# Optimization experiments

Measured on AMD Instinct MI355X. Metric: run time of the kernel, lower is better.

Reference implementation:

```python
import jax, jax.numpy as jnp
import numpy as np

N_TIME = 512          # n_time_nodes
LATENT = 32           # latent_dim
HIDDEN = 64           # hidden_dim
N_MODES = 8           # r_fourier_modes
X_A0 = 0.3            # initial stoichiometry (anode)
CSANMAX = 28700.0     # max concentration scale
BASE_LOGIT = float(np.log(X_A0 / (1.0 - X_A0)))  # logit_from_fraction(x_a0)
FEAT_DIM = 1 + 2 * N_MODES   # [rho, cos(k*pi*rho), sin(k*pi*rho)]
IN_DIM = LATENT + FEAT_DIM
N_POINTS = 2_000_000


def setup_inputs() -> dict:
    key = jax.random.key(0)
    ks = jax.random.split(key, 8)
    time_idx = jax.random.randint(ks[0], (N_POINTS,), 0, N_TIME)
    rho = jax.random.uniform(ks[1], (N_POINTS,), dtype=jnp.float32)
    # trainable latent code per nonzero time node
    emb = jax.random.normal(ks[2], (N_TIME - 1, LATENT), dtype=jnp.float32) * 0.02
    # decoder_a: Linear(IN,HID)+SiLU, Linear(HID,HID)+SiLU, Linear(HID,1)
    W0 = jax.random.normal(ks[3], (IN_DIM, HIDDEN), dtype=jnp.float32) / np.sqrt(IN_DIM)
    b0 = jnp.zeros((HIDDEN,), jnp.float32)
    W1 = jax.random.normal(ks[4], (HIDDEN, HIDDEN), dtype=jnp.float32) / np.sqrt(HIDDEN)
    b1 = jnp.zeros((HIDDEN,), jnp.float32)
    Wout = jax.random.normal(ks[5], (HIDDEN, 1), dtype=jnp.float32) * 0.1
    bout = jnp.zeros((1,), jnp.float32)
    return {"time_idx": time_idx, "rho": rho, "emb": emb,
            "W0": W0, "b0": b0, "W1": W1, "b1": b1, "Wout": Wout, "bout": bout}


def _radius_features(rho):
    # [N] -> [N, 1 + 2*N_MODES]
    k = jnp.arange(1, N_MODES + 1, dtype=rho.dtype)
    ang = jnp.pi * rho[:, None] * k[None, :]
    return jnp.concatenate([rho[:, None], jnp.cos(ang), jnp.sin(ang)], axis=1)


def reference(time_idx, rho, emb, W0, b0, W1, b1, Wout, bout):
    # predicated version of the torch masked scatter: compute everywhere,
    # select initial-condition value where time_idx == 0
    idx = jnp.clip(time_idx - 1, 0, N_TIME - 2)       # safe gather index
    e = emb[idx]                                       # [N, LATENT]
    feat = _radius_features(rho)                       # [N, FEAT_DIM]
    h = jnp.concatenate([e, feat], axis=1)             # [N, IN_DIM]
    h = jax.nn.silu(h @ W0 + b0)
    h = jax.nn.silu(h @ W1 + b1)
    raw = (h @ Wout + bout)[:, 0]                      # [N]
    theta = jax.nn.sigmoid(raw + BASE_LOGIT)
    return jnp.where(time_idx == 0, X_A0 * CSANMAX, theta * CSANMAX)
```

## Files before the change

kernel.cpp:

```cpp
#include <hip/hip_runtime.h>
#include <stdint.h>


typedef _Float16 half8  __attribute__((ext_vector_type(8)));
typedef _Float16 half4v __attribute__((ext_vector_type(4)));
typedef _Float16 half2v __attribute__((ext_vector_type(2)));
typedef float f32x4 __attribute__((ext_vector_type(4)));

#define LOG2E 1.44269504088896340736f
#define NLN2  -0.6931471805599453f
#define CSCL  -1.44269504088896340736f
#define BASE_LOGIT -0.84729786038720367f
#define CSANMAX 28700.0f
#define IC_VAL 8610.0f

__device__ __forceinline__ float fast_exp2(float x) { return __builtin_amdgcn_exp2f(x); }
__device__ __forceinline__ float fast_rcp(float x)  { return __builtin_amdgcn_rcpf(x); }
__device__ __forceinline__ void usilu2(float u0, float u1, float& p0, float& p1) {
  const float d0 = 1.0f + fast_exp2(u0);
  const float d1 = 1.0f + fast_exp2(u1);
  const float r  = fast_rcp(d0 * d1);
  p0 = u0 * d1 * r;
  p1 = u1 * d0 * r;
}
__device__ __forceinline__ half2v pkh(float a, float b) {
  return __builtin_bit_cast(half2v, __builtin_amdgcn_cvt_pkrtz(a, b));
}

union H8 { half8 v8; half2v v2[4]; half4v v4[2]; };
union H4 { half4v v4; half2v v2[2]; };

__global__ __launch_bounds__(256, 3) void mlp_kernel(
    const int* __restrict__ tix, const float* __restrict__ rho,
    const float* __restrict__ emb, const float* __restrict__ W0,
    const float* __restrict__ b0, const float* __restrict__ W1,
    const float* __restrict__ b1, const float* __restrict__ Wout,
    const float* __restrict__ bout, float* __restrict__ out, int ntiles)
{
  __shared__ __align__(16) _Float16 stage[2][2][4][64][8];

  const int tid  = threadIdx.x;
  const int wid  = tid >> 6;
  const int lane = tid & 63;
  const int m    = lane & 15;
  const int q    = lane >> 4;

  if (wid == 0) {
#pragma unroll
    for (int t = 0; t < 4; ++t) {
#pragma unroll
      for (int s = 0; s < 2; ++s) {
        half8 f0, f1;
#pragma unroll
        for (int j = 0; j < 8; ++j) {
          const int k = s * 32 + q * 8 + j;
          const int n = t * 16 + m;
          float v0;
          if (k < 32) {
            v0 = W0[k * 64 + n];
          } else {
            const int kn = k - 32;
            v0 = (kn < 16) ? W0[(33 + kn) * 64 + n]
               : (kn == 16) ? W0[32 * 64 + n]
               : (kn == 17) ? b0[n] : 0.0f;
          }
          f0[j] = (_Float16)(CSCL * v0);
          const int hm = (s * 2 + (j >> 2)) * 16 + q * 4 + (j & 3);
          f1[j] = (_Float16)W1[hm * 64 + n];
        }
        *(half8*)&stage[0][s][t][lane][0] = f0;
        *(half8*)&stage[1][s][t][lane][0] = f1;
      }
    }
  }

  half2v biash[8];
  half2v wouth[8];
#pragma unroll
  for (int t = 0; t < 4; ++t) {
    const f32x4 bv = *(const f32x4*)(b1 + t * 16 + q * 4);
    const f32x4 wv = *(const f32x4*)(Wout + t * 16 + q * 4);
    biash[t * 2]     = pkh(CSCL * bv[0], CSCL * bv[1]);
    biash[t * 2 + 1] = pkh(CSCL * bv[2], CSCL * bv[3]);
    wouth[t * 2]     = pkh(NLN2 * wv[0], NLN2 * wv[1]);
    wouth[t * 2 + 1] = pkh(NLN2 * wv[2], NLN2 * wv[3]);
  }
  const float boutBL = bout[0] + BASE_LOGIT;

  __syncthreads();

  half8 w0A[4], w0B[4], w1A[4], w1B[4];
#pragma unroll
  for (int t = 0; t < 4; ++t) {
    w0A[t] = *(const half8*)&stage[0][0][t][lane][0];
    w0B[t] = *(const half8*)&stage[0][1][t][lane][0];
    w1A[t] = *(const half8*)&stage[1][0][t][lane][0];
    w1B[t] = *(const half8*)&stage[1][1][t][lane][0];
  }

  const f32x4 z = {0.0f, 0.0f, 0.0f, 0.0f};
  const int S = gridDim.x * 4;

  int tg = blockIdx.x * 4 + wid;
  if (tg >= ntiles) return;
  const int lim = ntiles - 1;

  auto phase1 = [&](float rhp, half8 X0v, H8& Y0o, H8& Y1o) {
    const float rev = 0.5f * rhp;
    const float c1  = __builtin_amdgcn_cosf(rev);
    const float s1f = __builtin_amdgcn_sinf(rev);
    const float tc  = 2.0f * c1;
    const float x1v = (q == 0) ? c1 : ((q == 1) ? s1f : 0.0f);
    const float x0v = (q == 0) ? 1.0f : 0.0f;
    const float x2v = tc * x1v - x0v;
    const float x3v = tc * x2v - x1v;
    const float x4v = tc * x3v - x2v;
    const float x5v = tc * x4v - x3v;
    const float x6v = tc * x5v - x4v;
    const float x7v = tc * x6v - x5v;
    const float x8v = tc * x7v - x6v;
    H8 X1;
    X1.v2[0] = (q == 2) ? pkh(rhp, 1.0f) : pkh(x1v, x2v);
    X1.v2[1] = pkh(x3v, x4v);
    X1.v2[2] = pkh(x5v, x6v);
    X1.v2[3] = pkh(x7v, x8v);

    f32x4 acc[4];
#pragma unroll
    for (int t = 0; t < 4; ++t) {
      f32x4 a = __builtin_amdgcn_mfma_f32_16x16x32_f16(w0A[t], X0v, z, 0, 0, 0);
      a = __builtin_amdgcn_mfma_f32_16x16x32_f16(w0B[t], X1.v8, a, 0, 0, 0);
      acc[t] = a;
    }
    H4 hh[4];
#pragma unroll
    for (int t = 0; t < 4; ++t) {
      float p0, p1, p2, p3;
      usilu2(acc[t][0], acc[t][1], p0, p1);
      usilu2(acc[t][2], acc[t][3], p2, p3);
      hh[t].v2[0] = pkh(p0, p1);
      hh[t].v2[1] = pkh(p2, p3);
    }
    Y0o.v4[0] = hh[0].v4; Y0o.v4[1] = hh[1].v4;
    Y1o.v4[0] = hh[2].v4; Y1o.v4[1] = hh[3].v4;
  };

  auto phase2 = [&](const H8& Y0p, const H8& Y1p, int icP, int tgP) {
    f32x4 acc[4];
#pragma unroll
    for (int t = 0; t < 4; ++t) {
      f32x4 a = __builtin_amdgcn_mfma_f32_16x16x32_f16(w1A[t], Y0p.v8, z, 0, 0, 0);
      a = __builtin_amdgcn_mfma_f32_16x16x32_f16(w1B[t], Y1p.v8, a, 0, 0, 0);
      acc[t] = a;
    }
    float dA = 0.0f, dB = 0.0f;
#pragma unroll
    for (int t = 0; t < 4; ++t) {
      float p0, p1, p2, p3;
      const float u0 = (float)biash[t * 2][0]     + acc[t][0];
      const float u1 = (float)biash[t * 2][1]     + acc[t][1];
      const float u2 = (float)biash[t * 2 + 1][0] + acc[t][2];
      const float u3 = (float)biash[t * 2 + 1][1] + acc[t][3];
      usilu2(u0, u1, p0, p1);
      usilu2(u2, u3, p2, p3);
      dA = fmaf(p0, (float)wouth[t * 2][0],     dA);
      dB = fmaf(p1, (float)wouth[t * 2][1],     dB);
      dA = fmaf(p2, (float)wouth[t * 2 + 1][0], dA);
      dB = fmaf(p3, (float)wouth[t * 2 + 1][1], dB);
    }
    float dot = dA + dB;
    dot += __shfl_xor(dot, 16, 64);
    dot += __shfl_xor(dot, 32, 64);
    const float theta = fast_rcp(1.0f + fast_exp2(-LOG2E * (dot + boutBL)));
    const float val = (icP == 0) ? IC_VAL : theta * CSANMAX;
    if (q == 0) out[tgP * 16 + m] = val;
  };

  int   tC = tix[tg * 16 + m];
  float rC = rho[tg * 16 + m];
  const int tg1 = min(tg + S, lim);
  int   tN = tix[tg1 * 16 + m];
  float rN = rho[tg1 * 16 + m];
  H8 X0C;
  {
    const int idx = min(max(tC - 1, 0), 510);
    const float* e = emb + (size_t)idx * 32 + q * 8;
    const f32x4 e0 = *(const f32x4*)e;
    const f32x4 e1 = *(const f32x4*)(e + 4);
    X0C.v2[0] = pkh(e0[0], e0[1]); X0C.v2[1] = pkh(e0[2], e0[3]);
    X0C.v2[2] = pkh(e1[0], e1[1]); X0C.v2[3] = pkh(e1[2], e1[3]);
  }
  H8 Y0p, Y1p;
  phase1(rC, X0C.v8, Y0p, Y1p);
  int icP = tC, tgP = tg;
  {
    const int idx = min(max(tN - 1, 0), 510);
    const float* e = emb + (size_t)idx * 32 + q * 8;
    const f32x4 e0 = *(const f32x4*)e;
    const f32x4 e1 = *(const f32x4*)(e + 4);
    X0C.v2[0] = pkh(e0[0], e0[1]); X0C.v2[1] = pkh(e0[2], e0[3]);
    X0C.v2[2] = pkh(e1[0], e1[1]); X0C.v2[3] = pkh(e1[2], e1[3]);
  }
  tC = tN; rC = rN;
  {
    const int tg2 = min(tg + 2 * S, lim);
    tN = tix[tg2 * 16 + m];
    rN = rho[tg2 * 16 + m];
  }
  tg += S;

  while (tg < ntiles) {
    const int tg2 = min(tg + 2 * S, lim);
    const int   tQ = tix[tg2 * 16 + m];
    const float rQ = rho[tg2 * 16 + m];
    const int idxN = min(max(tN - 1, 0), 510);
    const float* ern = emb + (size_t)idxN * 32 + q * 8;
    const f32x4 eN0 = *(const f32x4*)ern;
    const f32x4 eN1 = *(const f32x4*)(ern + 4);

    phase2(Y0p, Y1p, icP, tgP);
    phase1(rC, X0C.v8, Y0p, Y1p);

    icP = tC; tgP = tg;
    X0C.v2[0] = pkh(eN0[0], eN0[1]); X0C.v2[1] = pkh(eN0[2], eN0[3]);
    X0C.v2[2] = pkh(eN1[0], eN1[1]); X0C.v2[3] = pkh(eN1[2], eN1[3]);
    tC = tN; rC = rN;
    tN = tQ; rN = rQ;
    tg += S;
  }

  phase2(Y0p, Y1p, icP, tgP);
}

extern "C" void kernel_launch(void* const* d_in, const int* in_sizes, int n_in,
                              void* d_out, int out_size, void* d_ws, size_t ws_size,
                              hipStream_t stream) {
  const int*   tix  = (const int*)d_in[0];
  const float* rho  = (const float*)d_in[1];
  const float* emb  = (const float*)d_in[2];
  const float* W0   = (const float*)d_in[3];
  const float* b0   = (const float*)d_in[4];
  const float* W1   = (const float*)d_in[5];
  const float* b1   = (const float*)d_in[6];
  const float* Wout = (const float*)d_in[7];
  const float* bout = (const float*)d_in[8];
  float* outp = (float*)d_out;

  const int n      = in_sizes[0];
  const int ntiles = n / 16;

  int grid = 1024;
  const int maxg = (ntiles + 3) / 4;
  if (grid > maxg) grid = maxg;
  mlp_kernel<<<dim3(grid), dim3(256), 0, stream>>>(
      tix, rho, emb, W0, b0, W1, b1, Wout, bout, outp, ntiles);
}
```

Baseline: 163.0 us.

## Batch SiLU reciprocals, use MFMA for output dot, shorten prefetch pipeline

The SiLU helper now handles four values with one reciprocal instead of two values per reciprocal, cutting transcendental work. The final hidden-to-output dot product becomes two MFMA instructions with the output bias folded into the accumulator, replacing scalar FMAs and cross-lane shuffles. The index and rho prefetch depth drops from two tiles ahead to one, which frees registers but leaves the dependent embedding gather less latency to hide. Batching four values into one reciprocal adds some risk of overflow in the product of denominators.

```diff
diff --git a/kernel.cpp b/kernel.cpp
--- a/kernel.cpp
+++ b/kernel.cpp
@@ -16,12 +16,17 @@
 
 __device__ __forceinline__ float fast_exp2(float x) { return __builtin_amdgcn_exp2f(x); }
 __device__ __forceinline__ float fast_rcp(float x)  { return __builtin_amdgcn_rcpf(x); }
-__device__ __forceinline__ void usilu2(float u0, float u1, float& p0, float& p1) {
+__device__ __forceinline__ void usilu4(float u0, float u1, float u2, float u3,
+                                       float& p0, float& p1, float& p2, float& p3) {
   const float d0 = 1.0f + fast_exp2(u0);
   const float d1 = 1.0f + fast_exp2(u1);
-  const float r  = fast_rcp(d0 * d1);
-  p0 = u0 * d1 * r;
-  p1 = u1 * d0 * r;
+  const float d2 = 1.0f + fast_exp2(u2);
+  const float d3 = 1.0f + fast_exp2(u3);
+  const float d01 = d0 * d1, d23 = d2 * d3;
+  const float r   = fast_rcp(d01 * d23);
+  const float t01 = d23 * r, t23 = d01 * r;
+  p0 = u0 * d1 * t01;  p1 = u1 * d0 * t01;
+  p2 = u2 * d3 * t23;  p3 = u3 * d2 * t23;
 }
 __device__ __forceinline__ half2v pkh(float a, float b) {
   return __builtin_bit_cast(half2v, __builtin_amdgcn_cvt_pkrtz(a, b));
@@ -75,17 +80,23 @@
   }
 
   half2v biash[8];
-  half2v wouth[8];
 #pragma unroll
   for (int t = 0; t < 4; ++t) {
     const f32x4 bv = *(const f32x4*)(b1 + t * 16 + q * 4);
-    const f32x4 wv = *(const f32x4*)(Wout + t * 16 + q * 4);
     biash[t * 2]     = pkh(CSCL * bv[0], CSCL * bv[1]);
     biash[t * 2 + 1] = pkh(CSCL * bv[2], CSCL * bv[3]);
-    wouth[t * 2]     = pkh(NLN2 * wv[0], NLN2 * wv[1]);
-    wouth[t * 2 + 1] = pkh(NLN2 * wv[2], NLN2 * wv[3]);
+  }
+  H8 wdA, wdB;
+#pragma unroll
+  for (int a = 0; a < 4; ++a) {
+    const int j0 = 2 * a, j1 = 2 * a + 1;
+    const int h0 = ((j0 >> 2) * 16) + q * 4 + (j0 & 3);
+    const int h1 = ((j1 >> 2) * 16) + q * 4 + (j1 & 3);
+    wdA.v2[a] = pkh(NLN2 * Wout[h0],      NLN2 * Wout[h1]);
+    wdB.v2[a] = pkh(NLN2 * Wout[32 + h0], NLN2 * Wout[32 + h1]);
   }
   const float boutBL = bout[0] + BASE_LOGIT;
+  const f32x4 cBL = {boutBL, boutBL, boutBL, boutBL};
 
   __syncthreads();
 
@@ -136,8 +147,7 @@
 #pragma unroll
     for (int t = 0; t < 4; ++t) {
       float p0, p1, p2, p3;
-      usilu2(acc[t][0], acc[t][1], p0, p1);
-      usilu2(acc[t][2], acc[t][3], p2, p3);
+      usilu4(acc[t][0], acc[t][1], acc[t][2], acc[t][3], p0, p1, p2, p3);
       hh[t].v2[0] = pkh(p0, p1);
       hh[t].v2[1] = pkh(p2, p3);
     }
@@ -153,25 +163,24 @@
       a = __builtin_amdgcn_mfma_f32_16x16x32_f16(w1B[t], Y1p.v8, a, 0, 0, 0);
       acc[t] = a;
     }
-    float dA = 0.0f, dB = 0.0f;
-#pragma unroll
-    for (int t = 0; t < 4; ++t) {
-      float p0, p1, p2, p3;
+    H4 hh2[4];
+#pragma unroll
+    for (int t = 0; t < 4; ++t) {
       const float u0 = (float)biash[t * 2][0]     + acc[t][0];
       const float u1 = (float)biash[t * 2][1]     + acc[t][1];
       const float u2 = (float)biash[t * 2 + 1][0] + acc[t][2];
       const float u3 = (float)biash[t * 2 + 1][1] + acc[t][3];
-      usilu2(u0, u1, p0, p1);
-      usilu2(u2, u3, p2, p3);
-      dA = fmaf(p0, (float)wouth[t * 2][0],     dA);
-      dB = fmaf(p1, (float)wouth[t * 2][1],     dB);
-      dA = fmaf(p2, (float)wouth[t * 2 + 1][0], dA);
-      dB = fmaf(p3, (float)wouth[t * 2 + 1][1], dB);
-    }
-    float dot = dA + dB;
-    dot += __shfl_xor(dot, 16, 64);
-    dot += __shfl_xor(dot, 32, 64);
-    const float theta = fast_rcp(1.0f + fast_exp2(-LOG2E * (dot + boutBL)));
+      float p0, p1, p2, p3;
+      usilu4(u0, u1, u2, u3, p0, p1, p2, p3);
+      hh2[t].v2[0] = pkh(p0, p1);
+      hh2[t].v2[1] = pkh(p2, p3);
+    }
+    H8 B0, B1;
+    B0.v4[0] = hh2[0].v4; B0.v4[1] = hh2[1].v4;
+    B1.v4[0] = hh2[2].v4; B1.v4[1] = hh2[3].v4;
+    f32x4 d2 = __builtin_amdgcn_mfma_f32_16x16x32_f16(wdA.v8, B0.v8, cBL, 0, 0, 0);
+    d2 = __builtin_amdgcn_mfma_f32_16x16x32_f16(wdB.v8, B1.v8, d2, 0, 0, 0);
+    const float theta = fast_rcp(1.0f + fast_exp2(-LOG2E * d2[0]));
     const float val = (icP == 0) ? IC_VAL : theta * CSANMAX;
     if (q == 0) out[tgP * 16 + m] = val;
   };
@@ -202,18 +211,13 @@
     X0C.v2[2] = pkh(e1[0], e1[1]); X0C.v2[3] = pkh(e1[2], e1[3]);
   }
   tC = tN; rC = rN;
-  {
-    const int tg2 = min(tg + 2 * S, lim);
-    tN = tix[tg2 * 16 + m];
-    rN = rho[tg2 * 16 + m];
-  }
   tg += S;
 
   while (tg < ntiles) {
-    const int tg2 = min(tg + 2 * S, lim);
-    const int   tQ = tix[tg2 * 16 + m];
-    const float rQ = rho[tg2 * 16 + m];
-    const int idxN = min(max(tN - 1, 0), 510);
+    const int tgn = min(tg + S, lim);
+    const int   tQ = tix[tgn * 16 + m];
+    const float rQ = rho[tgn * 16 + m];
+    const int idxN = min(max(tQ - 1, 0), 510);
     const float* ern = emb + (size_t)idxN * 32 + q * 8;
     const f32x4 eN0 = *(const f32x4*)ern;
     const f32x4 eN1 = *(const f32x4*)(ern + 4);
@@ -224,8 +228,7 @@
     icP = tC; tgP = tg;
     X0C.v2[0] = pkh(eN0[0], eN0[1]); X0C.v2[1] = pkh(eN0[2], eN0[3]);
     X0C.v2[2] = pkh(eN1[0], eN1[1]); X0C.v2[3] = pkh(eN1[2], eN1[3]);
-    tC = tN; rC = rN;
-    tN = tQ; rN = rQ;
+    tC = tQ; rC = rQ;
     tg += S;
   }
 
```

Measured after the change: 165.8 us. Within noise of the previous version (+1.7%).
